# Kernel optimization log

Measured on AMD Instinct MI355X. Metric: run time of the kernel, lower is better.

The kernel has to match this reference:

```python
import jax, jax.numpy as jnp
import numpy as np
from jax import lax

SIGMA = 10.0


def _maxpool3(x):
    # x: (1, N, D, H, W), kernel 3, stride 1, VALID
    return lax.reduce_window(x, -jnp.inf, lax.max,
                             (1, 1, 3, 3, 3), (1, 1, 1, 1, 1), 'VALID')


def _avgpool3(x):
    s = lax.reduce_window(x, 0.0, lax.add,
                          (1, 1, 3, 3, 3), (1, 1, 1, 1, 1), 'VALID')
    return s / 27.0


def _smooth(x):
    # ReplicationPad3d(3) -> MaxPool3d(3,1) -> AvgPool3d(3,1) x2 ; keeps spatial size
    x = jnp.pad(x, ((0, 0), (0, 0), (3, 3), (3, 3), (3, 3)), mode='edge')
    return _avgpool3(_avgpool3(_maxpool3(x)))


def setup_inputs() -> dict:
    key = jax.random.key(0)
    k1, k2, k3 = jax.random.split(key, 3)
    N, K, L = 10000, 8, 13
    cost = jax.random.normal(k1, (N, 1, L, L, L), dtype=jnp.float32)
    knn = jax.random.randint(k2, (N, K), 0, N)
    dist_nn = jax.random.uniform(k3, (N, K), dtype=jnp.float32) * 20.0
    alpha = jnp.array([1.0, 0.1, 1.0, 1.0, 0.1, 1.0], dtype=jnp.float32)
    return {"cost": cost, "knn": knn, "dist_nn": dist_nn, "alpha": alpha}


def reference(cost, knn, dist_nn, alpha):
    N = cost.shape[0]
    L = cost.shape[2]
    cost = alpha[1] + alpha[0] * cost                       # (N,1,L,L,L)
    w = jnp.exp(-dist_nn / (2.0 * SIGMA ** 2))              # (N,K)
    norm = w.sum(axis=1)                                    # (N,)
    cost = cost.reshape(1, N, L, L, L)

    cost_approx = _smooth(cost)                             # (1,N,L,L,L)
    # gather K neighbors and do distance-weighted mean
    nbr = cost_approx[:, knn]                               # (1,N,K,L,L,L)
    cost_approx = jnp.einsum('ankxyz,nk->anxyz', nbr, w)
    cost_approx = cost_approx / norm[None, :, None, None, None]

    cost = alpha[4] + alpha[2] * cost + alpha[3] * cost_approx
    cost = _smooth(cost)
    nbr = cost[:, knn]                                      # (1,N,K,L,L,L)
    cost = jnp.einsum('ankxyz,nk->anxyz', nbr, w)
    cost = cost / norm[None, :, None, None, None]
    return alpha[5] * cost.reshape(1, N, -1)
```

## Files before the change

kernel.cpp:

```cpp
#include <hip/hip_runtime.h>
#include <math.h>

#define L3 2197
#define SP 2200
#define NV (SP / 8)
#define NTS 320
#define NTO 320

#define SSZ 4913

typedef unsigned int u32;

__device__ __forceinline__ u32 pack2bf(float a, float b) {
    u32 ua = __float_as_uint(a);
    u32 ub = __float_as_uint(b);
    ua = (ua + 0x7fffu + ((ua >> 16) & 1u)) >> 16;
    ub = (ub + 0x7fffu + ((ub >> 16) & 1u)) & 0xffff0000u;
    return ua | ub;
}

__device__ __forceinline__ void unpack8(uint4 v, float* f) {
    f[0] = __uint_as_float(v.x << 16);
    f[1] = __uint_as_float(v.x & 0xffff0000u);
    f[2] = __uint_as_float(v.y << 16);
    f[3] = __uint_as_float(v.y & 0xffff0000u);
    f[4] = __uint_as_float(v.z << 16);
    f[5] = __uint_as_float(v.z & 0xffff0000u);
    f[6] = __uint_as_float(v.w << 16);
    f[7] = __uint_as_float(v.w & 0xffff0000u);
}

__device__ __forceinline__ uint4 pack8(const float* f) {
    uint4 v;
    v.x = pack2bf(f[0], f[1]);
    v.y = pack2bf(f[2], f[3]);
    v.z = pack2bf(f[4], f[5]);
    v.w = pack2bf(f[6], f[7]);
    return v;
}

__device__ __forceinline__ void maxpool_row(const float* x, float* o) {
    float p[12];
#pragma unroll
    for (int i = 0; i < 12; ++i) p[i] = fmaxf(x[i], x[i + 1]);
    o[0] = x[0];
    o[1] = x[0];
    o[2] = p[0];
#pragma unroll
    for (int j = 3; j <= 13; ++j) o[j] = fmaxf(p[j - 3], x[j - 1]);
    o[14] = p[11];
    o[15] = x[12];
    o[16] = x[12];
}

__device__ __forceinline__ void tri_row(const float* y, float* o, float scale) {
#pragma unroll
    for (int c = 0; c < 13; ++c) {
        float s = fmaf(2.0f, y[c + 1], y[c]);
        s = fmaf(3.0f, y[c + 2], s);
        s = fmaf(2.0f, y[c + 3], s);
        o[c] = (s + y[c + 4]) * scale;
    }
}

__device__ void smooth_single(float* S, int tid) {
    __syncthreads();
    {
        const bool act = tid < 169;
        float x[13], o[17];
        if (act) {
            const float* src = S + tid * 13;
#pragma unroll
            for (int i = 0; i < 13; ++i) x[i] = src[i];
            maxpool_row(x, o);
        }
        __syncthreads();
        if (act) {
            float* d = S + tid * 17;
#pragma unroll
            for (int i = 0; i < 17; ++i) d[i] = o[i];
        }
        __syncthreads();
    }
    {
        const bool act = tid < 221;
        const int a = tid / 17, c = tid % 17;
        float x[13], o[17];
        if (act) {
            const float* src = S + a * 221 + c;
#pragma unroll
            for (int i = 0; i < 13; ++i) x[i] = src[i * 17];
            maxpool_row(x, o);
        }
        __syncthreads();
        if (act) {
            float* d = S + a * 289 + c;
#pragma unroll
            for (int i = 0; i < 17; ++i) d[i * 17] = o[i];
        }
        __syncthreads();
    }
    if (tid < 289) {
        float x[13], m[17], o[13];
        const float* src = S + tid;
#pragma unroll
        for (int i = 0; i < 13; ++i) x[i] = src[i * 289];
        maxpool_row(x, m);
        tri_row(m, o, 1.0f);
        float* d = S + tid;
#pragma unroll
        for (int i = 0; i < 13; ++i) d[i * 289] = o[i];
    }
    __syncthreads();
    {
        const bool act = tid < 221;
        const int a = tid / 17, c = tid % 17;
        float y[17], o[13];
        if (act) {
            const float* src = S + a * 289 + c;
#pragma unroll
            for (int i = 0; i < 17; ++i) y[i] = src[i * 17];
            tri_row(y, o, 1.0f);
        }
        __syncthreads();
        if (act) {
            float* d = S + a * 221 + c;
#pragma unroll
            for (int i = 0; i < 13; ++i) d[i * 17] = o[i];
        }
        __syncthreads();
    }
    {
        const bool act = tid < 169;
        float y[17], o[13];
        if (act) {
            const float* src = S + tid * 17;
#pragma unroll
            for (int i = 0; i < 17; ++i) y[i] = src[i];
            tri_row(y, o, 1.0f / 729.0f);
        }
        __syncthreads();
        if (act) {
            float* d = S + tid * 13;
#pragma unroll
            for (int i = 0; i < 13; ++i) d[i] = o[i];
        }
        __syncthreads();
    }
}

__device__ __forceinline__ void load_nbr_meta(
        const int* __restrict__ knn, const float* __restrict__ dist,
        int n, int K, int* idx, float* wk, float* norm_out) {
    float dv[8];
#pragma unroll
    for (int k = 0; k < 8; ++k) {
        const int kc = (k < K) ? k : (K - 1);
        idx[k] = knn[n * K + kc];
        dv[k] = dist[n * K + kc];
    }
    float norm = 0.0f;
#pragma unroll
    for (int k = 0; k < 8; ++k) {
        float w = (k < K) ? expf(-dv[k] * (1.0f / 200.0f)) : 0.0f;
        wk[k] = w;
        norm += w;
    }
    *norm_out = norm;
}

__global__ __launch_bounds__(NTS) void k_smooth1(
        const float* __restrict__ cost, const float* __restrict__ alpha,
        uint4* __restrict__ tmp1, uint4* __restrict__ preA) {
    __shared__ alignas(16) float S[SSZ];
    const int n = blockIdx.x;
    const int tid = threadIdx.x;
    const float a0 = alpha[0], a1 = alpha[1], a2 = alpha[2], a4 = alpha[4];
    const float* src = cost + (size_t)n * L3;
    for (int i = tid; i < L3; i += NTS) S[i] = fmaf(a0, src[i], a1);
    if (tid < SP - L3) S[L3 + tid] = 0.0f;
    __syncthreads();
    uint4* pre = preA + (size_t)n * NV;
    if (tid < NV) {
        float f[8];
#pragma unroll
        for (int j = 0; j < 8; ++j) f[j] = fmaf(a2, S[8 * tid + j], a4);
        pre[tid] = pack8(f);
    }
    smooth_single(S, tid);
    uint4* dst = tmp1 + (size_t)n * NV;
    if (tid < NV) {
        float f[8];
        const int base = 8 * tid;
#pragma unroll
        for (int j = 0; j < 8; ++j) f[j] = (base + j < L3) ? S[base + j] : 0.0f;
        dst[tid] = pack8(f);
    }
}

__global__ __launch_bounds__(NTS) void k_mid(
        const int* __restrict__ knn, const float* __restrict__ dist,
        const float* __restrict__ alpha, const uint4* __restrict__ tmp1,
        const uint4* __restrict__ preA, uint4* __restrict__ tmp2, int K) {
    __shared__ alignas(16) float S[SSZ];
    const int n = blockIdx.x;
    const int tid = threadIdx.x;
    int idx[8];
    float wk[8], norm;
    load_nbr_meta(knn, dist, n, K, idx, wk, &norm);
    const float sc = alpha[3] / norm;

    if (tid < NV) {
        uint4 v[8];
        const uint4 pv = preA[(size_t)n * NV + tid];
#pragma unroll
        for (int k = 0; k < 8; ++k) {
            const size_t b = (size_t)__builtin_amdgcn_readfirstlane(idx[k]) * NV;
            v[k] = tmp1[b + tid];
        }
        float f[8], acc[8], g[8];
        unpack8(pv, f);
#pragma unroll
        for (int j = 0; j < 8; ++j) acc[j] = 0.0f;
#pragma unroll
        for (int k = 0; k < 8; ++k) {
            unpack8(v[k], g);
#pragma unroll
            for (int j = 0; j < 8; ++j) acc[j] = fmaf(wk[k], g[j], acc[j]);
        }
#pragma unroll
        for (int j = 0; j < 8; ++j) S[8 * tid + j] = fmaf(sc, acc[j], f[j]);
    }
    smooth_single(S, tid);
    uint4* dst = tmp2 + (size_t)n * NV;
    if (tid < NV) {
        float f[8];
        const int base = 8 * tid;
#pragma unroll
        for (int j = 0; j < 8; ++j) f[j] = (base + j < L3) ? S[base + j] : 0.0f;
        dst[tid] = pack8(f);
    }
}

__global__ __launch_bounds__(NTO) void k_out(
        const int* __restrict__ knn, const float* __restrict__ dist,
        const float* __restrict__ alpha, const uint4* __restrict__ tmp2,
        float* __restrict__ out, int K) {
    const int n = blockIdx.x;
    const int tid = threadIdx.x;
    int idx[8];
    float wk[8], norm;
    load_nbr_meta(knn, dist, n, K, idx, wk, &norm);
    const float sc = alpha[5] / norm;

    float* dst = out + (size_t)n * L3;
    if (tid < NV) {
        uint4 v[8];
#pragma unroll
        for (int k = 0; k < 8; ++k) {
            const size_t b = (size_t)__builtin_amdgcn_readfirstlane(idx[k]) * NV;
            v[k] = tmp2[b + tid];
        }
        float acc[8], g[8];
#pragma unroll
        for (int j = 0; j < 8; ++j) acc[j] = 0.0f;
#pragma unroll
        for (int k = 0; k < 8; ++k) {
            unpack8(v[k], g);
#pragma unroll
            for (int j = 0; j < 8; ++j) acc[j] = fmaf(wk[k], g[j], acc[j]);
        }
        const int base = 8 * tid;
#pragma unroll
        for (int j = 0; j < 8; ++j)
            if (base + j < L3) dst[base + j] = sc * acc[j];
    }
}

extern "C" void kernel_launch(void* const* d_in, const int* in_sizes, int n_in,
                              void* d_out, int out_size, void* d_ws, size_t ws_size,
                              hipStream_t stream) {
    const float* cost  = (const float*)d_in[0];
    const int*   knn   = (const int*)d_in[1];
    const float* dist  = (const float*)d_in[2];
    const float* alpha = (const float*)d_in[3];
    float* out = (float*)d_out;

    const int N = in_sizes[0] / L3;
    int K = in_sizes[1] / N;
    if (K > 8) K = 8;

    uint4* tmp1 = (uint4*)d_ws;
    uint4* tmp2 = tmp1 + (size_t)N * NV;
    uint4* preA = tmp2 + (size_t)N * NV;

    k_smooth1<<<N, NTS, 0, stream>>>(cost, alpha, tmp1, preA);
    k_mid<<<N, NTS, 0, stream>>>(knn, dist, alpha, tmp1, preA, tmp2, K);
    k_out<<<N, NTO, 0, stream>>>(knn, dist, alpha, tmp2, out, K);
}
```

Before: 331.4 us.

## Run smoothing kernels as single-wave blocks and software-pipeline neighbor gathers

The first two kernels now launch one 64-lane wavefront per point instead of 320 threads. Each wave loops over the row and column chunks of every smoothing pass, which removes the idle lanes of the old mapping (169, 221 or 289 active out of 320). Most block-wide barriers become scheduling barriers, and the shared buffer is trimmed to the largest intermediate so more blocks fit per CU. In k_mid the neighbor gather prefetches the next chunk's nine loads while the current chunk is accumulated. The trade-off is more serial work per wave and higher register pressure from the double-buffered loads.

```diff
diff --git a/kernel.cpp b/kernel.cpp
--- a/kernel.cpp
+++ b/kernel.cpp
@@ -4,10 +4,10 @@
 #define L3 2197
 #define SP 2200
 #define NV (SP / 8)
-#define NTS 320
+#define NTW 64
 #define NTO 320
 
-#define SSZ 4913
+#define SSZ 3760
 
 typedef unsigned int u32;
 
@@ -63,90 +63,106 @@
     }
 }
 
-__device__ void smooth_single(float* S, int tid) {
-    __syncthreads();
-    {
-        const bool act = tid < 169;
+__device__ void smooth_wave(float* S, const int lane) {
+    __syncthreads();
+#pragma unroll
+    for (int cb = 2; cb >= 0; --cb) {
+        const int p = cb * 64 + lane;
+        const bool act = p < 169;
         float x[13], o[17];
         if (act) {
-            const float* src = S + tid * 13;
-#pragma unroll
-            for (int i = 0; i < 13; ++i) x[i] = src[i];
+            const float* s = S + p * 13;
+#pragma unroll
+            for (int i = 0; i < 13; ++i) x[i] = s[i];
             maxpool_row(x, o);
         }
-        __syncthreads();
-        if (act) {
-            float* d = S + tid * 17;
+        __builtin_amdgcn_sched_barrier(0);
+        if (act) {
+            float* d = S + p * 17;
 #pragma unroll
             for (int i = 0; i < 17; ++i) d[i] = o[i];
         }
-        __syncthreads();
-    }
-    {
-        const bool act = tid < 221;
-        const int a = tid / 17, c = tid % 17;
+        __builtin_amdgcn_sched_barrier(0);
+    }
+    __syncthreads();
+#pragma unroll
+    for (int cb = 3; cb >= 0; --cb) {
+        const int p = cb * 64 + lane;
+        const bool act = p < 221;
+        const int a = p / 17, c = p % 17;
         float x[13], o[17];
         if (act) {
-            const float* src = S + a * 221 + c;
-#pragma unroll
-            for (int i = 0; i < 13; ++i) x[i] = src[i * 17];
+            const float* s = S + a * 221 + c;
+#pragma unroll
+            for (int i = 0; i < 13; ++i) x[i] = s[i * 17];
             maxpool_row(x, o);
         }
-        __syncthreads();
+        __builtin_amdgcn_sched_barrier(0);
         if (act) {
             float* d = S + a * 289 + c;
 #pragma unroll
             for (int i = 0; i < 17; ++i) d[i * 17] = o[i];
         }
-        __syncthreads();
-    }
-    if (tid < 289) {
-        float x[13], m[17], o[13];
-        const float* src = S + tid;
-#pragma unroll
-        for (int i = 0; i < 13; ++i) x[i] = src[i * 289];
-        maxpool_row(x, m);
-        tri_row(m, o, 1.0f);
-        float* d = S + tid;
-#pragma unroll
-        for (int i = 0; i < 13; ++i) d[i * 289] = o[i];
-    }
-    __syncthreads();
-    {
-        const bool act = tid < 221;
-        const int a = tid / 17, c = tid % 17;
+        __builtin_amdgcn_sched_barrier(0);
+    }
+    __syncthreads();
+#pragma unroll
+    for (int cb = 0; cb < 5; ++cb) {
+        const int p = cb * 64 + lane;
+        if (p < 289) {
+            float x[13], m[17], o[13];
+            const float* s = S + p;
+#pragma unroll
+            for (int i = 0; i < 13; ++i) x[i] = s[i * 289];
+            maxpool_row(x, m);
+            tri_row(m, o, 1.0f);
+            float* d = S + p;
+#pragma unroll
+            for (int i = 0; i < 13; ++i) d[i * 289] = o[i];
+        }
+    }
+    __syncthreads();
+#pragma unroll
+    for (int cb = 0; cb < 4; ++cb) {
+        const int p = cb * 64 + lane;
+        const bool act = p < 221;
+        const int a = p / 17, c = p % 17;
         float y[17], o[13];
         if (act) {
-            const float* src = S + a * 289 + c;
-#pragma unroll
-            for (int i = 0; i < 17; ++i) y[i] = src[i * 17];
+            const float* s = S + a * 289 + c;
+#pragma unroll
+            for (int i = 0; i < 17; ++i) y[i] = s[i * 17];
             tri_row(y, o, 1.0f);
         }
-        __syncthreads();
+        __builtin_amdgcn_sched_barrier(0);
         if (act) {
             float* d = S + a * 221 + c;
 #pragma unroll
             for (int i = 0; i < 13; ++i) d[i * 17] = o[i];
         }
-        __syncthreads();
-    }
-    {
-        const bool act = tid < 169;
+        __builtin_amdgcn_sched_barrier(0);
+    }
+    __syncthreads();
+#pragma unroll
+    for (int cb = 0; cb < 3; ++cb) {
+        const int p = cb * 64 + lane;
+        const bool act = p < 169;
         float y[17], o[13];
         if (act) {
-            const float* src = S + tid * 17;
-#pragma unroll
-            for (int i = 0; i < 17; ++i) y[i] = src[i];
+            const float* s = S + p * 17;
+#pragma unroll
+            for (int i = 0; i < 17; ++i) y[i] = s[i];
             tri_row(y, o, 1.0f / 729.0f);
         }
-        __syncthreads();
-        if (act) {
-            float* d = S + tid * 13;
+        __builtin_amdgcn_sched_barrier(0);
+        if (act) {
+            float* d = S + p * 13;
 #pragma unroll
             for (int i = 0; i < 13; ++i) d[i] = o[i];
         }
-        __syncthreads();
-    }
+        __builtin_amdgcn_sched_barrier(0);
+    }
+    __syncthreads();
 }
 
 __device__ __forceinline__ void load_nbr_meta(
@@ -169,76 +185,107 @@
     *norm_out = norm;
 }
 
-__global__ __launch_bounds__(NTS) void k_smooth1(
+__global__ __launch_bounds__(NTW) void k_smooth1(
         const float* __restrict__ cost, const float* __restrict__ alpha,
         uint4* __restrict__ tmp1, uint4* __restrict__ preA) {
     __shared__ alignas(16) float S[SSZ];
     const int n = blockIdx.x;
-    const int tid = threadIdx.x;
+    const int lane = threadIdx.x;
     const float a0 = alpha[0], a1 = alpha[1], a2 = alpha[2], a4 = alpha[4];
     const float* src = cost + (size_t)n * L3;
-    for (int i = tid; i < L3; i += NTS) S[i] = fmaf(a0, src[i], a1);
-    if (tid < SP - L3) S[L3 + tid] = 0.0f;
+    for (int i = lane; i < L3; i += NTW) S[i] = fmaf(a0, src[i], a1);
+    if (lane < SP - L3) S[L3 + lane] = 0.0f;
     __syncthreads();
     uint4* pre = preA + (size_t)n * NV;
-    if (tid < NV) {
-        float f[8];
-#pragma unroll
-        for (int j = 0; j < 8; ++j) f[j] = fmaf(a2, S[8 * tid + j], a4);
-        pre[tid] = pack8(f);
-    }
-    smooth_single(S, tid);
+#pragma unroll
+    for (int r = 0; r < 5; ++r) {
+        const int i = r * 64 + lane;
+        if (i < NV) {
+            float f[8];
+#pragma unroll
+            for (int j = 0; j < 8; ++j) f[j] = fmaf(a2, S[8 * i + j], a4);
+            pre[i] = pack8(f);
+        }
+    }
+    smooth_wave(S, lane);
     uint4* dst = tmp1 + (size_t)n * NV;
-    if (tid < NV) {
-        float f[8];
-        const int base = 8 * tid;
-#pragma unroll
-        for (int j = 0; j < 8; ++j) f[j] = (base + j < L3) ? S[base + j] : 0.0f;
-        dst[tid] = pack8(f);
-    }
-}
-
-__global__ __launch_bounds__(NTS) void k_mid(
+#pragma unroll
+    for (int r = 0; r < 5; ++r) {
+        const int i = r * 64 + lane;
+        if (i < NV) {
+            float f[8];
+            const int base = 8 * i;
+#pragma unroll
+            for (int j = 0; j < 8; ++j) f[j] = (base + j < L3) ? S[base + j] : 0.0f;
+            dst[i] = pack8(f);
+        }
+    }
+}
+
+__global__ __launch_bounds__(NTW) void k_mid(
         const int* __restrict__ knn, const float* __restrict__ dist,
         const float* __restrict__ alpha, const uint4* __restrict__ tmp1,
         const uint4* __restrict__ preA, uint4* __restrict__ tmp2, int K) {
     __shared__ alignas(16) float S[SSZ];
     const int n = blockIdx.x;
-    const int tid = threadIdx.x;
+    const int lane = threadIdx.x;
     int idx[8];
     float wk[8], norm;
     load_nbr_meta(knn, dist, n, K, idx, wk, &norm);
     const float sc = alpha[3] / norm;
 
-    if (tid < NV) {
-        uint4 v[8];
-        const uint4 pv = preA[(size_t)n * NV + tid];
-#pragma unroll
-        for (int k = 0; k < 8; ++k) {
-            const size_t b = (size_t)__builtin_amdgcn_readfirstlane(idx[k]) * NV;
-            v[k] = tmp1[b + tid];
-        }
-        float f[8], acc[8], g[8];
-        unpack8(pv, f);
-#pragma unroll
-        for (int j = 0; j < 8; ++j) acc[j] = 0.0f;
-#pragma unroll
-        for (int k = 0; k < 8; ++k) {
-            unpack8(v[k], g);
-#pragma unroll
-            for (int j = 0; j < 8; ++j) acc[j] = fmaf(wk[k], g[j], acc[j]);
-        }
-#pragma unroll
-        for (int j = 0; j < 8; ++j) S[8 * tid + j] = fmaf(sc, acc[j], f[j]);
-    }
-    smooth_single(S, tid);
+    const uint4* pre = preA + (size_t)n * NV;
+    const uint4* nb[8];
+#pragma unroll
+    for (int k = 0; k < 8; ++k)
+        nb[k] = tmp1 + (size_t)__builtin_amdgcn_readfirstlane(idx[k]) * NV;
+
+    uint4 av[9], bv[9];
+    {
+        const int i = lane;
+        av[8] = pre[i];
+#pragma unroll
+        for (int k = 0; k < 8; ++k) av[k] = nb[k][i];
+    }
+#pragma unroll
+    for (int r = 0; r < 5; ++r) {
+        if (r < 4) {
+            const int i = (r + 1) * 64 + lane;
+            const int ic = (i < NV) ? i : (NV - 1);
+            bv[8] = pre[ic];
+#pragma unroll
+            for (int k = 0; k < 8; ++k) bv[k] = nb[k][ic];
+        }
+        const int i = r * 64 + lane;
+        if (i < NV) {
+            float f[8], acc[8], g[8];
+            unpack8(av[8], f);
+#pragma unroll
+            for (int j = 0; j < 8; ++j) acc[j] = 0.0f;
+#pragma unroll
+            for (int k = 0; k < 8; ++k) {
+                unpack8(av[k], g);
+#pragma unroll
+                for (int j = 0; j < 8; ++j) acc[j] = fmaf(wk[k], g[j], acc[j]);
+            }
+#pragma unroll
+            for (int j = 0; j < 8; ++j) S[8 * i + j] = fmaf(sc, acc[j], f[j]);
+        }
+#pragma unroll
+        for (int q = 0; q < 9; ++q) av[q] = bv[q];
+    }
+    smooth_wave(S, lane);
     uint4* dst = tmp2 + (size_t)n * NV;
-    if (tid < NV) {
-        float f[8];
-        const int base = 8 * tid;
-#pragma unroll
-        for (int j = 0; j < 8; ++j) f[j] = (base + j < L3) ? S[base + j] : 0.0f;
-        dst[tid] = pack8(f);
+#pragma unroll
+    for (int r = 0; r < 5; ++r) {
+        const int i = r * 64 + lane;
+        if (i < NV) {
+            float f[8];
+            const int base = 8 * i;
+#pragma unroll
+            for (int j = 0; j < 8; ++j) f[j] = (base + j < L3) ? S[base + j] : 0.0f;
+            dst[i] = pack8(f);
+        }
     }
 }
 
@@ -294,7 +341,7 @@
     uint4* tmp2 = tmp1 + (size_t)N * NV;
     uint4* preA = tmp2 + (size_t)N * NV;
 
-    k_smooth1<<<N, NTS, 0, stream>>>(cost, alpha, tmp1, preA);
-    k_mid<<<N, NTS, 0, stream>>>(knn, dist, alpha, tmp1, preA, tmp2, K);
+    k_smooth1<<<N, NTW, 0, stream>>>(cost, alpha, tmp1, preA);
+    k_mid<<<N, NTW, 0, stream>>>(knn, dist, alpha, tmp1, preA, tmp2, K);
     k_out<<<N, NTO, 0, stream>>>(knn, dist, alpha, tmp2, out, K);
 }
```

After: 339.4 us. 2.4% more time.
